# Kernel tuning notes

Hardware: AMD Instinct MI355X
Metric: run time of the kernel (lower is better)

## Reference

```python
import jax, jax.numpy as jnp
import numpy as np

N_EMBD = 1024
N_HEAD = 16
HEAD_DIM = N_EMBD // N_HEAD


def setup_inputs() -> dict:
    key = jax.random.key(0)
    k1, k2, k3, k4, k5 = jax.random.split(key, 5)
    x = jax.random.normal(k1, (4, 2048, N_EMBD), dtype=jnp.float32)
    s_in = 1.0 / np.sqrt(N_EMBD)
    W_attn = jax.random.normal(k2, (N_EMBD, 3 * N_EMBD), dtype=jnp.float32) * s_in
    b_attn = jax.random.normal(k3, (3 * N_EMBD,), dtype=jnp.float32) * 0.01
    W_proj = jax.random.normal(k4, (N_EMBD, N_EMBD), dtype=jnp.float32) * s_in
    b_proj = jax.random.normal(k5, (N_EMBD,), dtype=jnp.float32) * 0.01
    return {"x": x, "W_attn": W_attn, "b_attn": b_attn, "W_proj": W_proj, "b_proj": b_proj}


def reference(x, W_attn, b_attn, W_proj, b_proj):
    B, T, C = x.shape
    qkv = jnp.einsum('btc,cd->btd', x, W_attn) + b_attn  # [B,T,3C]
    q, k, v = jnp.split(qkv, 3, axis=2)
    # [B,T,C] -> [B,H,T,Dh]
    def heads(t):
        return t.reshape(B, T, N_HEAD, HEAD_DIM).transpose(0, 2, 1, 3)
    q, k, v = heads(q), heads(k), heads(v)
    scale = HEAD_DIM ** -0.5
    att = jnp.einsum('bhqd,bhkd->bhqk', q, k) * scale  # [B,H,T,T]
    causal = jnp.tril(jnp.ones((T, T), dtype=bool))
    att = jnp.where(causal[None, None], att, -jnp.inf)
    att = jax.nn.softmax(att, axis=-1)
    y = jnp.einsum('bhqk,bhkd->bhqd', att, v)  # [B,H,T,Dh]
    y = y.transpose(0, 2, 1, 3).reshape(B, T, C)
    y = jnp.einsum('btc,cd->btd', y, W_proj) + b_proj
    return y
```

## Files before the change

### kernel.cpp

```cpp
#include <hip/hip_runtime.h>

typedef unsigned short u16;
typedef unsigned int u32;
typedef __bf16 bf16x8 __attribute__((ext_vector_type(8)));
typedef u16 u16x8 __attribute__((ext_vector_type(8)));
typedef u16 u16x4 __attribute__((ext_vector_type(4)));
typedef float f32x4 __attribute__((ext_vector_type(4)));
typedef float f32x16 __attribute__((ext_vector_type(16)));

#define BHTD 8388608
#define QSCALE 0.18033688f
#define SMAX 16.0f

__device__ __forceinline__ u16 f2bf(float f) {
  union { float f; u32 u; } x; x.f = f;
  u32 r = (x.u + 0x7FFFu + ((x.u >> 16) & 1u)) >> 16;
  return (u16)r;
}

__device__ __forceinline__ u32 cvt_pk_bf16(float lo, float hi) {
  u32 r;
  asm("v_cvt_pk_bf16_f32 %0, %1, %2" : "=v"(r) : "v"(lo), "v"(hi));
  return r;
}

__device__ __forceinline__ void permlane32_swap(u32& x, u32& y) {
  asm("v_permlane32_swap_b32 %0, %1" : "+v"(x), "+v"(y));
}

__device__ __forceinline__ void async_copy16(const u16* gsrc, u16* ldst) {
  __builtin_amdgcn_global_load_lds(
      (const __attribute__((address_space(1))) void*)gsrc,
      (__attribute__((address_space(3))) void*)ldst, 16, 0, 0);
}

#define MF(a, b, c) __builtin_amdgcn_mfma_f32_16x16x32_bf16((a), (b), (c), 0, 0, 0)

__global__ __launch_bounds__(256) void conv_x_kernel(const float4* __restrict__ in,
                                                     u16x4* __restrict__ out, int n4) {
  int i = blockIdx.x * 256 + threadIdx.x;
  int stride = gridDim.x * 256;
  for (; i < n4; i += stride) {
    float4 v = in[i];
    u16x4 o = { f2bf(v.x), f2bf(v.y), f2bf(v.z), f2bf(v.w) };
    out[i] = o;
  }
}

__global__ __launch_bounds__(256) void transpose_bf16(const float* __restrict__ W,
                                                      u16* __restrict__ Wt, int K, int N) {
  __shared__ float t[64][65];
  int c0 = blockIdx.x * 64;
  int r0 = blockIdx.y * 64;
  int c = threadIdx.x & 63;
  int r4 = threadIdx.x >> 6;
#pragma unroll
  for (int j = 0; j < 16; ++j) {
    int r = j * 4 + r4;
    t[r][c] = W[(size_t)(r0 + r) * N + (c0 + c)];
  }
  __syncthreads();
#pragma unroll
  for (int j = 0; j < 16; ++j) {
    int n = j * 4 + r4;
    Wt[(size_t)(c0 + n) * K + (r0 + c)] = f2bf(t[c][n]);
  }
}

template <int MODE>
__global__ __launch_bounds__(512, 2) void gemm_bf16(const u16* __restrict__ A,
                                                    const u16* __restrict__ Bt,
                                                    const float* __restrict__ bias,
                                                    float* __restrict__ outp,
                                                    u16* __restrict__ qkv, int grid_n) {
  __shared__ __attribute__((aligned(16))) u16 Al[3][256 * 64];
  __shared__ __attribute__((aligned(16))) u16 Bl[3][128 * 64];
  const int tid = threadIdx.x;
  const int lane = tid & 63, wave = tid >> 6;
  const int wr = wave >> 1, wc = wave & 1;
  const int bn = blockIdx.x % grid_n, bm = blockIdx.x / grid_n;
  const int m0 = bm * 256, n0 = bn * 128;
  const int g = lane >> 4, c16 = lane & 15;
  const int xs = c16 & 7;
  const int offK0 = ((g ^ xs) << 3);
  const int offK1 = (((4 + g) ^ xs) << 3);

#define STAGE_A_(t, s, c)                                                         \
  {                                                                               \
    int row_ = (c) >> 3, sl_ = (c) & 7;                                           \
    async_copy16(&A[(size_t)(m0 + row_) * 1024 + (t) * 64 + ((sl_ ^ (row_ & 7)) << 3)], \
                 &Al[s][(c) << 3]);                                               \
  }
#define STAGE_B_(t, s, c)                                                         \
  {                                                                               \
    int row_ = (c) >> 3, sl_ = (c) & 7;                                           \
    async_copy16(&Bt[(size_t)(n0 + row_) * 1024 + (t) * 64 + ((sl_ ^ (row_ & 7)) << 3)], \
                 &Bl[s][(c) << 3]);                                               \
  }

  f32x4 acc[4][4] = {};
  bf16x8 aF[2][4][2], bF[2][4][2];

#pragma unroll
  for (int t = 0; t < 3; ++t) {
    STAGE_B_(t, t, tid); STAGE_B_(t, t, tid + 512);
    STAGE_A_(t, t, tid); STAGE_A_(t, t, tid + 512);
    STAGE_A_(t, t, tid + 1024); STAGE_A_(t, t, tid + 1536);
  }
  asm volatile("s_waitcnt vmcnt(12)" ::: "memory");
  __builtin_amdgcn_s_barrier();
#pragma unroll
  for (int m = 0; m < 4; ++m) {
    int row = wr * 64 + m * 16 + c16;
    aF[0][m][0] = *(const bf16x8*)&Al[0][row * 64 + offK0];
    aF[0][m][1] = *(const bf16x8*)&Al[0][row * 64 + offK1];
  }
#pragma unroll
  for (int n = 0; n < 4; ++n) {
    int row = wc * 64 + n * 16 + c16;
    bF[0][n][0] = *(const bf16x8*)&Bl[0][row * 64 + offK0];
    bF[0][n][1] = *(const bf16x8*)&Bl[0][row * 64 + offK1];
  }
  asm volatile("s_waitcnt lgkmcnt(0)" ::: "memory");
  __builtin_amdgcn_s_barrier();

#pragma unroll
  for (int j = 0; j < 16; ++j) {
    const int cur = j & 1, nxt = cur ^ 1;
    const int sR = (j + 1) % 3;
    const int sW = j % 3;
    const bool rd = (j < 15);
    const bool st = (j < 13);

    if (j <= 13) {
      asm volatile("s_waitcnt vmcnt(6)" ::: "memory");
    } else if (j == 14) {
      asm volatile("s_waitcnt vmcnt(0)" ::: "memory");
    }
    __builtin_amdgcn_s_barrier();

    if (rd) {
#pragma unroll
      for (int m = 0; m < 4; ++m) {
        int row = wr * 64 + m * 16 + c16;
        aF[nxt][m][0] = *(const bf16x8*)&Al[sR][row * 64 + offK0];
        aF[nxt][m][1] = *(const bf16x8*)&Al[sR][row * 64 + offK1];
      }
#pragma unroll
      for (int n = 0; n < 4; ++n) {
        int row = wc * 64 + n * 16 + c16;
        bF[nxt][n][0] = *(const bf16x8*)&Bl[sR][row * 64 + offK0];
        bF[nxt][n][1] = *(const bf16x8*)&Bl[sR][row * 64 + offK1];
      }
    }
    if (st) { STAGE_B_(j + 3, sW, tid); STAGE_B_(j + 3, sW, tid + 512); }
    __builtin_amdgcn_s_setprio(1);
#pragma unroll
    for (int m = 0; m < 4; ++m)
#pragma unroll
      for (int n = 0; n < 4; ++n) acc[m][n] = MF(aF[cur][m][0], bF[cur][n][0], acc[m][n]);
    __builtin_amdgcn_s_setprio(0);
    __builtin_amdgcn_s_barrier();

    if (st) {
      STAGE_A_(j + 3, sW, tid); STAGE_A_(j + 3, sW, tid + 512);
      STAGE_A_(j + 3, sW, tid + 1024); STAGE_A_(j + 3, sW, tid + 1536);
    }
    __builtin_amdgcn_s_setprio(1);
#pragma unroll
    for (int m = 0; m < 4; ++m)
#pragma unroll
      for (int n = 0; n < 4; ++n) acc[m][n] = MF(aF[cur][m][1], bF[cur][n][1], acc[m][n]);
    __builtin_amdgcn_s_setprio(0);
    __builtin_amdgcn_s_barrier();
  }

  float bv[4];
#pragma unroll
  for (int nb = 0; nb < 4; ++nb) bv[nb] = bias[n0 + wc * 64 + nb * 16 + c16];

#pragma unroll
  for (int mb = 0; mb < 4; ++mb) {
    int row0 = m0 + wr * 64 + mb * 16 + g * 4;
#pragma unroll
    for (int nb = 0; nb < 4; ++nb) {
      int col = n0 + wc * 64 + nb * 16 + c16;
      float bvn = bv[nb];
      if (MODE == 0) {
        int sel = col >> 10, ci = col & 1023;
        int hh = ci >> 6, d = ci & 63;
        int bb = row0 >> 11, t0 = row0 & 2047;
        float qs = (sel == 0) ? QSCALE : 1.0f;
        if (sel == 2) {
          u16x4 pk;
#pragma unroll
          for (int r = 0; r < 4; ++r) pk[r] = f2bf(acc[mb][nb][r] + bvn);
          *(u16x4*)&qkv[(size_t)2 * BHTD + (((size_t)(bb * 16 + hh) * 64 + d) << 11) + t0] = pk;
        } else {
#pragma unroll
          for (int r = 0; r < 4; ++r) {
            qkv[(size_t)sel * BHTD + (((size_t)(bb * 16 + hh) * 2048 + t0 + r) << 6) + d] =
                f2bf((acc[mb][nb][r] + bvn) * qs);
          }
        }
      } else {
#pragma unroll
        for (int r = 0; r < 4; ++r)
          outp[((size_t)(row0 + r) << 10) + col] = acc[mb][nb][r] + bvn;
      }
    }
  }
#undef STAGE_A_
#undef STAGE_B_
}

__global__ __launch_bounds__(256, 4) void attn_fwd(const u16* __restrict__ Q,
                                                   const u16* __restrict__ K,
                                                   const u16* __restrict__ VT,
                                                   u16* __restrict__ Y) {
  __shared__ __attribute__((aligned(16))) u16 KV[2][2][64 * 64];
  float* Pl = (float*)&KV[0][0][0];
  float* Ll = (float*)&KV[1][0][0];
  const float NEG_BIG = -1e30f;

  int bid = blockIdx.x;
  int qt = 31 - (bid >> 6), hd = bid & 63;
  size_t hb = (size_t)hd * (2048 * 64);
  const u16* Qh = Q + hb;
  const u16* Kh = K + hb;
  const u16* Vh = VT + hb;
  int tid = threadIdx.x, lane = tid & 63, w = tid >> 6;
  int rg = w & 1, par = w >> 1;
  int c32 = lane & 31, h = lane >> 5;
  const int xs = c32 & 7;
  const int qrow = qt * 64 + rg * 32 + c32;

  int ch0 = tid, ch1 = tid + 256;
  int sr0 = ch0 >> 3, sw0 = ((ch0 & 7) ^ (sr0 & 7)) << 3;
  int sr1 = ch1 >> 3, sw1 = ((ch1 & 7) ^ (sr1 & 7)) << 3;

  bf16x8 qf[4];
#pragma unroll
  for (int dk = 0; dk < 4; ++dk)
    qf[dk] = *(const bf16x8*)&Qh[(size_t)qrow * 64 + dk * 16 + 8 * h];

  async_copy16(&Kh[(size_t)sr0 * 64 + sw0], &KV[0][0][ch0 << 3]);
  async_copy16(&Kh[(size_t)sr1 * 64 + sw1], &KV[0][0][ch1 << 3]);
  async_copy16(&Vh[(size_t)sr0 * 2048 + sw0], &KV[0][1][ch0 << 3]);
  async_copy16(&Vh[(size_t)sr1 * 2048 + sw1], &KV[0][1][ch1 << 3]);

  float l = 0.f;
  f32x16 o0 = {}, o1 = {};

  for (int it = 0; it <= qt; ++it) {
    int cb = it & 1;
    __syncthreads();

    if (it < qt) {
      int kv1 = (it + 1) << 6;
      async_copy16(&Kh[(size_t)(kv1 + sr0) * 64 + sw0], &KV[cb ^ 1][0][ch0 << 3]);
      async_copy16(&Kh[(size_t)(kv1 + sr1) * 64 + sw1], &KV[cb ^ 1][0][ch1 << 3]);
      async_copy16(&Vh[(size_t)sr0 * 2048 + kv1 + sw0], &KV[cb ^ 1][1][ch0 << 3]);
      async_copy16(&Vh[(size_t)sr1 * 2048 + kv1 + sw1], &KV[cb ^ 1][1][ch1 << 3]);
    }

    const bool lastit = (it == qt);
    if (!(lastit && rg == 0 && par == 1)) {
      const int kv0 = (it << 6) + par * 32;

      bf16x8 kf[4];
#pragma unroll
      for (int dk = 0; dk < 4; ++dk)
        kf[dk] = *(const bf16x8*)&KV[cb][0][(par * 32 + c32) * 64 + (((2 * dk + h) ^ xs) << 3)];
      f32x16 s0;
#pragma unroll
      for (int i = 0; i < 16; ++i) s0[i] = -SMAX;
      __builtin_amdgcn_s_setprio(1);
#pragma unroll
      for (int dk = 0; dk < 4; ++dk)
        s0 = __builtin_amdgcn_mfma_f32_32x32x16_bf16(kf[dk], qf[dk], s0, 0, 0, 0);
      __builtin_amdgcn_s_setprio(0);

      if (lastit) {
        int kvb = kv0 + 4 * h;
#pragma unroll
        for (int reg = 0; reg < 16; ++reg) {
          int kvl = kvb + 8 * (reg >> 2) + (reg & 3);
          if (kvl > qrow) s0[reg] = NEG_BIG;
        }
      }

#pragma unroll
      for (int i = 0; i < 16; ++i) s0[i] = __builtin_exp2f(s0[i]);
      float b0 = s0[0] + s0[4], b1 = s0[1] + s0[5], b2 = s0[2] + s0[6], b3 = s0[3] + s0[7];
      b0 += s0[8] + s0[12]; b1 += s0[9] + s0[13]; b2 += s0[10] + s0[14]; b3 += s0[11] + s0[15];
      float rs = (b0 + b1) + (b2 + b3);
      rs += __shfl_xor(rs, 32);
      l += rs;

      u32 pw0[8];
#pragma unroll
      for (int mm = 0; mm < 8; ++mm) pw0[mm] = cvt_pk_bf16(s0[2 * mm], s0[2 * mm + 1]);
      permlane32_swap(pw0[0], pw0[2]); permlane32_swap(pw0[1], pw0[3]);
      permlane32_swap(pw0[4], pw0[6]); permlane32_swap(pw0[5], pw0[7]);

      __builtin_amdgcn_s_setprio(1);
#pragma unroll
      for (int c = 0; c < 2; ++c) {
        const int a = 4 * c;
        union { u32 u[4]; bf16x8 v; } pf;
        pf.u[0] = pw0[a + 0]; pf.u[1] = pw0[a + 1];
        pf.u[2] = pw0[a + 2]; pf.u[3] = pw0[a + 3];
        int slot = ((4 * par + 2 * c + h) ^ xs) << 3;
        bf16x8 vfa = *(const bf16x8*)&KV[cb][1][c32 * 64 + slot];
        bf16x8 vfb = *(const bf16x8*)&KV[cb][1][(32 + c32) * 64 + slot];
        o0 = __builtin_amdgcn_mfma_f32_32x32x16_bf16(vfa, pf.v, o0, 0, 0, 0);
        o1 = __builtin_amdgcn_mfma_f32_32x32x16_bf16(vfb, pf.v, o1, 0, 0, 0);
      }
      __builtin_amdgcn_s_setprio(0);
    }
  }

  __syncthreads();

  if (par == 1) {
#pragma unroll
    for (int db = 0; db < 2; ++db)
#pragma unroll
      for (int rq = 0; rq < 4; ++rq)
#pragma unroll
        for (int jj = 0; jj < 4; ++jj) {
          int d = db * 32 + 8 * rq + 4 * h + jj;
          Pl[rg * 2048 + d * 32 + c32] = (db ? o1[rq * 4 + jj] : o0[rq * 4 + jj]);
        }
    if (h == 0) Ll[rg * 32 + c32] = l;
  }
  __syncthreads();
  if (par == 0) {
    float lt = l + Ll[rg * 32 + c32];
    float inv = 1.0f / lt;
    size_t yb =
        (size_t)(hd >> 4) * (2048 * 1024) + (size_t)(hd & 15) * 64 + (size_t)qrow * 1024;
#pragma unroll
    for (int db = 0; db < 2; ++db)
#pragma unroll
      for (int rq = 0; rq < 4; ++rq) {
        u16x4 pk;
#pragma unroll
        for (int jj = 0; jj < 4; ++jj) {
          int d = db * 32 + 8 * rq + 4 * h + jj;
          float v = (db ? o1[rq * 4 + jj] : o0[rq * 4 + jj]) + Pl[rg * 2048 + d * 32 + c32];
          pk[jj] = f2bf(v * inv);
        }
        *(u16x4*)&Y[yb + db * 32 + 8 * rq + 4 * h] = pk;
      }
  }
}

extern "C" void kernel_launch(void* const* d_in, const int* in_sizes, int n_in,
                              void* d_out, int out_size, void* d_ws, size_t ws_size,
                              hipStream_t stream) {
  (void)in_sizes; (void)n_in; (void)out_size; (void)ws_size;
  const float* x      = (const float*)d_in[0];
  const float* W_attn = (const float*)d_in[1];
  const float* b_attn = (const float*)d_in[2];
  const float* W_proj = (const float*)d_in[3];
  const float* b_proj = (const float*)d_in[4];
  float* out = (float*)d_out;

  char* ws = (char*)d_ws;
  u16* Xb  = (u16*)(ws);
  u16* Wt  = (u16*)(ws + 16777216);
  u16* Wpt = (u16*)(ws + 16777216 + 6291456);
  u16* QKV = (u16*)(ws + 16777216 + 6291456 + 2097152);
  u16* Yb  = Xb;

  conv_x_kernel<<<2048, 256, 0, stream>>>((const float4*)x, (u16x4*)Xb, 2097152);
  transpose_bf16<<<dim3(48, 16), 256, 0, stream>>>(W_attn, Wt, 1024, 3072);
  transpose_bf16<<<dim3(16, 16), 256, 0, stream>>>(W_proj, Wpt, 1024, 1024);
  gemm_bf16<0><<<768, 512, 0, stream>>>(Xb, Wt, b_attn, nullptr, QKV, 24);
  attn_fwd<<<2048, 256, 0, stream>>>(QKV, QKV + BHTD, QKV + 2 * BHTD, Yb);
  gemm_bf16<1><<<256, 512, 0, stream>>>(Yb, Wpt, b_proj, out, nullptr, 8);
}
```

Before: 158.5 us.

## Load GEMM A fragments directly from global into registers, drop A LDS staging

The GEMM no longer stages the A tile through shared memory. Each wave loads its A fragments straight from global memory into registers one k-step ahead, so A rows are now read with strided per-lane loads instead of coalesced async copies. This frees 96KB of LDS and removes the mid-iteration barrier, reworking the vmcnt waits to match. The risk is that A reads are less coalesced, A data is re-read by the two column waves, and global latency is hidden only one step ahead.

```diff
diff --git a/kernel.cpp b/kernel.cpp
--- a/kernel.cpp
+++ b/kernel.cpp
@@ -73,7 +73,6 @@
                                                     const float* __restrict__ bias,
                                                     float* __restrict__ outp,
                                                     u16* __restrict__ qkv, int grid_n) {
-  __shared__ __attribute__((aligned(16))) u16 Al[3][256 * 64];
   __shared__ __attribute__((aligned(16))) u16 Bl[3][128 * 64];
   const int tid = threadIdx.x;
   const int lane = tid & 63, wave = tid >> 6;
@@ -85,12 +84,6 @@
   const int offK0 = ((g ^ xs) << 3);
   const int offK1 = (((4 + g) ^ xs) << 3);
 
-#define STAGE_A_(t, s, c)                                                         \
-  {                                                                               \
-    int row_ = (c) >> 3, sl_ = (c) & 7;                                           \
-    async_copy16(&A[(size_t)(m0 + row_) * 1024 + (t) * 64 + ((sl_ ^ (row_ & 7)) << 3)], \
-                 &Al[s][(c) << 3]);                                               \
-  }
 #define STAGE_B_(t, s, c)                                                         \
   {                                                                               \
     int row_ = (c) >> 3, sl_ = (c) & 7;                                           \
@@ -98,31 +91,31 @@
                  &Bl[s][(c) << 3]);                                               \
   }
 
+  const u16* Ab[4];
+#pragma unroll
+  for (int m = 0; m < 4; ++m)
+    Ab[m] = A + ((size_t)(m0 + wr * 64 + m * 16 + c16) << 10) + 8 * g;
+
   f32x4 acc[4][4] = {};
   bf16x8 aF[2][4][2], bF[2][4][2];
 
-#pragma unroll
-  for (int t = 0; t < 3; ++t) {
-    STAGE_B_(t, t, tid); STAGE_B_(t, t, tid + 512);
-    STAGE_A_(t, t, tid); STAGE_A_(t, t, tid + 512);
-    STAGE_A_(t, t, tid + 1024); STAGE_A_(t, t, tid + 1536);
+  STAGE_B_(0, 0, tid); STAGE_B_(0, 0, tid + 512);
+  STAGE_B_(1, 1, tid); STAGE_B_(1, 1, tid + 512);
+  STAGE_B_(2, 2, tid); STAGE_B_(2, 2, tid + 512);
+  __builtin_amdgcn_sched_barrier(0);
+#pragma unroll
+  for (int m = 0; m < 4; ++m) {
+    aF[0][m][0] = *(const bf16x8*)&Ab[m][0];
+    aF[0][m][1] = *(const bf16x8*)&Ab[m][32];
   }
   asm volatile("s_waitcnt vmcnt(12)" ::: "memory");
   __builtin_amdgcn_s_barrier();
-#pragma unroll
-  for (int m = 0; m < 4; ++m) {
-    int row = wr * 64 + m * 16 + c16;
-    aF[0][m][0] = *(const bf16x8*)&Al[0][row * 64 + offK0];
-    aF[0][m][1] = *(const bf16x8*)&Al[0][row * 64 + offK1];
-  }
 #pragma unroll
   for (int n = 0; n < 4; ++n) {
     int row = wc * 64 + n * 16 + c16;
     bF[0][n][0] = *(const bf16x8*)&Bl[0][row * 64 + offK0];
     bF[0][n][1] = *(const bf16x8*)&Bl[0][row * 64 + offK1];
   }
-  asm volatile("s_waitcnt lgkmcnt(0)" ::: "memory");
-  __builtin_amdgcn_s_barrier();
 
 #pragma unroll
   for (int j = 0; j < 16; ++j) {
@@ -132,19 +125,23 @@
     const bool rd = (j < 15);
     const bool st = (j < 13);
 
-    if (j <= 13) {
-      asm volatile("s_waitcnt vmcnt(6)" ::: "memory");
+    if (j == 0) {
+      asm volatile("s_waitcnt vmcnt(10)" ::: "memory");
+    } else if (j <= 13) {
+      asm volatile("s_waitcnt vmcnt(18)" ::: "memory");
     } else if (j == 14) {
-      asm volatile("s_waitcnt vmcnt(0)" ::: "memory");
-    }
-    __builtin_amdgcn_s_barrier();
+      asm volatile("s_waitcnt vmcnt(16)" ::: "memory");
+    }
+    if (j < 15) __builtin_amdgcn_s_barrier();
+
+    if (st) { STAGE_B_(j + 3, sW, tid); STAGE_B_(j + 3, sW, tid + 512); }
+    __builtin_amdgcn_sched_barrier(0);
 
     if (rd) {
 #pragma unroll
       for (int m = 0; m < 4; ++m) {
-        int row = wr * 64 + m * 16 + c16;
-        aF[nxt][m][0] = *(const bf16x8*)&Al[sR][row * 64 + offK0];
-        aF[nxt][m][1] = *(const bf16x8*)&Al[sR][row * 64 + offK1];
+        aF[nxt][m][0] = *(const bf16x8*)&Ab[m][(j + 1) * 64];
+        aF[nxt][m][1] = *(const bf16x8*)&Ab[m][(j + 1) * 64 + 32];
       }
 #pragma unroll
       for (int n = 0; n < 4; ++n) {
@@ -153,26 +150,17 @@
         bF[nxt][n][1] = *(const bf16x8*)&Bl[sR][row * 64 + offK1];
       }
     }
-    if (st) { STAGE_B_(j + 3, sW, tid); STAGE_B_(j + 3, sW, tid + 512); }
+
     __builtin_amdgcn_s_setprio(1);
 #pragma unroll
     for (int m = 0; m < 4; ++m)
 #pragma unroll
       for (int n = 0; n < 4; ++n) acc[m][n] = MF(aF[cur][m][0], bF[cur][n][0], acc[m][n]);
-    __builtin_amdgcn_s_setprio(0);
-    __builtin_amdgcn_s_barrier();
-
-    if (st) {
-      STAGE_A_(j + 3, sW, tid); STAGE_A_(j + 3, sW, tid + 512);
-      STAGE_A_(j + 3, sW, tid + 1024); STAGE_A_(j + 3, sW, tid + 1536);
-    }
-    __builtin_amdgcn_s_setprio(1);
 #pragma unroll
     for (int m = 0; m < 4; ++m)
 #pragma unroll
       for (int n = 0; n < 4; ++n) acc[m][n] = MF(aF[cur][m][1], bF[cur][n][1], acc[m][n]);
     __builtin_amdgcn_s_setprio(0);
-    __builtin_amdgcn_s_barrier();
   }
 
   float bv[4];
@@ -210,7 +198,6 @@
       }
     }
   }
-#undef STAGE_A_
 #undef STAGE_B_
 }
 
```

Result: slower. 229.7 us (+44.9%).
